# Kernel tuning notes

Measured on AMD Instinct MI355X. Metric: run time of the kernel, lower is better.

Reference implementation:

```python
import jax, jax.numpy as jnp
import numpy as np

INV_SQRT2 = 0.7071067811865476
BETA = 0.3
LN_EPS = 1e-5

B, S, P, C, TD = 128, 1024, 336, 128, 4
H1, H2, K = C // 4, C // 8, 3  # rda=4, rdb=8, ksize=3


def setup_inputs() -> dict:
    key = jax.random.key(0)
    ks = jax.random.split(key, 20)
    rn = lambda k, sh: jax.random.normal(k, sh, dtype=jnp.float32)
    return {
        "x": rn(ks[0], (B, S, C)),
        "x_mark_enc": rn(ks[1], (B, S, TD)),
        "x_dec": rn(ks[2], (B, P, C)),
        "y_mark_dec": rn(ks[3], (B, P, TD)),
        # time_enc params
        "W1": rn(ks[4], (H1, TD)) * 0.1, "b1": jnp.zeros((H1,), jnp.float32),
        "g1": jnp.ones((H1,), jnp.float32), "be1": jnp.zeros((H1,), jnp.float32),
        "W2": rn(ks[5], (H2, H1)) * 0.1, "b2": jnp.zeros((H2,), jnp.float32),
        "g2": jnp.ones((H2,), jnp.float32), "be2": jnp.zeros((H2,), jnp.float32),
        "Wc": rn(ks[6], (S, S, K)) * 0.02, "bc": jnp.zeros((S,), jnp.float32),
        "W3": rn(ks[7], (C, H2)) * 0.1, "b3": jnp.zeros((C,), jnp.float32),
        # projections
        "Wtp": rn(ks[8], (P, S)) * 0.02, "btp": jnp.zeros((P,), jnp.float32),
        "Whp": rn(ks[9], (P, S)) * 0.02, "bhp": jnp.zeros((P,), jnp.float32),
    }


def _haar_level1(x):
    # pywt.wavedec(sig, 'db1', level=1) -> [cA, cD]; concat along time.
    # For even length: cA[k]=(x[2k]+x[2k+1])/sqrt(2), cD[k]=(x[2k]-x[2k+1])/sqrt(2).
    xe, xo = x[:, 0::2, :], x[:, 1::2, :]
    cA = (xe + xo) * INV_SQRT2
    cD = (xe - xo) * INV_SQRT2
    return jnp.concatenate([cA, cD], axis=1)  # [B, S, C]


def _layernorm(h, g, b):
    m = jnp.mean(h, axis=-1, keepdims=True)
    v = jnp.mean((h - m) ** 2, axis=-1, keepdims=True)
    return (h - m) * jax.lax.rsqrt(v + LN_EPS) * g + b


def reference(x, x_mark_enc, x_dec, y_mark_dec,
              W1, b1, g1, be1, W2, b2, g2, be2, Wc, bc, W3, b3,
              Wtp, btp, Whp, bhp):
    # wavelet transform + instance norm over time (torch.var is unbiased)
    xw = _haar_level1(x)
    means = jnp.mean(xw, axis=1, keepdims=True)
    stdev = jnp.sqrt(jnp.var(xw, axis=1, ddof=1, keepdims=True) + 1e-5)
    xn = (xw - means) / stdev

    # time_enc MLP: Linear -> LN -> ReLU -> Linear -> LN -> ReLU
    h = jax.nn.relu(_layernorm(jnp.einsum('bst,ht->bsh', x_mark_enc, W1) + b1, g1, be1))
    h = jax.nn.relu(_layernorm(jnp.einsum('bsh,gh->bsg', h, W2) + b2, g2, be2))
    # Conv1d(in=seq_len, out=seq_len, k=3, padding='same') over feature dim H2
    h = jax.lax.conv_general_dilated(h, Wc, window_strides=(1,), padding='SAME',
                                     dimension_numbers=('NCH', 'OIH', 'NCH'))
    h = h + bc[None, :, None]
    time_embed = jnp.einsum('bsg,cg->bsc', h, W3) + b3  # [B, S, C]

    # seq->pred projections (Linear over time axis), then blend
    time_out = jnp.einsum('bsc,ps->bpc', time_embed, Wtp) + btp[None, :, None]
    pred = jnp.einsum('bsc,ps->bpc', xn, Whp) + bhp[None, :, None]
    pred = BETA * pred + (1.0 - BETA) * time_out
    pred = pred * stdev + means
    return pred  # [B, P, C] == dec_out[:, -pred_len:, :]
```

## Files before the change

kernel.cpp:

```cpp
#include <hip/hip_runtime.h>
#include <hip/hip_bf16.h>

#define INV_SQRT2f 0.70710678118654752440f
#define BETAf 0.3f
#define OMBf  0.7f
#define LN_EPSf 1e-5f

#define B 128
#define S 1024
#define P 336
#define C 128
#define H1 32
#define H2 16

#define WS_WHP2G  0
#define WS_EPI    262144
#define WS_BCP    296448
#define WS_H2     296832
#define WS_M      2393984
#define WS_AIMG   3426176

typedef short  s16x8 __attribute__((ext_vector_type(8)));
typedef float  f32x4 __attribute__((ext_vector_type(4)));

__device__ __forceinline__ unsigned f2bf(float f) {
    unsigned u = __float_as_uint(f);
    return (u + 0x7fffu + ((u >> 16) & 1u)) >> 16;
}

__device__ __forceinline__ int whp2l_u32(int p, int sp) {
    int kt   = sp >> 4;
    int tile = kt * 2 + p / 192;
    int sub  = (p % 192) >> 4;
    int kg   = (sp & 15) >> 2;
    int m    = p & 15;
    int byte = tile * 12288 + sub * 1024 + kg * 256 + m * 16 + 4 * (sp & 3);
    return byte >> 2;
}

__global__ void k_prep(const float* __restrict__ Whp, const float* __restrict__ Wtp,
                       const float* __restrict__ bc,  const float* __restrict__ bhp,
                       const float* __restrict__ btp, float* __restrict__ ws)
{
    const int p = blockIdx.x;
    const int t = threadIdx.x;
    unsigned* img = (unsigned*)ws;
    __shared__ float red[768];
    float sw = 0.f, rw = 0.f, bp = 0.f;
    for (int sp = t; sp < 512; sp += 256) {
        float a = Whp[p * 1024 + sp];
        float d = Whp[p * 1024 + 512 + sp];
        float va = BETAf * (a + d) * INV_SQRT2f;
        float vb = BETAf * (a - d) * INV_SQRT2f;
        img[whp2l_u32(p, sp)] = f2bf(va) | (f2bf(vb) << 16);
        sw += a + d;
    }
    for (int s = t; s < S; s += 256) {
        float w = Wtp[p * 1024 + s];
        rw += w;
        bp += w * bc[s];
    }
    red[t] = sw; red[256 + t] = rw; red[512 + t] = bp;
    __syncthreads();
    for (int off = 128; off > 0; off >>= 1) {
        if (t < off) {
            red[t]       += red[t + off];
            red[256 + t] += red[256 + t + off];
            red[512 + t] += red[512 + t + off];
        }
        __syncthreads();
    }
    if (t == 0) {
        ws[WS_BCP + p] = red[512];
        float* e = ws + WS_EPI + p * 4;
        e[0] = BETAf * bhp[p] + OMBf * btp[p];
        e[1] = OMBf * red[256];
        e[2] = 1.f - BETAf * red[0];
        e[3] = 0.f;
    }
}

__global__ void k_mlp(const float* __restrict__ xme,
                      const float* __restrict__ W1, const float* __restrict__ b1,
                      const float* __restrict__ g1, const float* __restrict__ be1,
                      const float* __restrict__ W2, const float* __restrict__ b2,
                      const float* __restrict__ g2, const float* __restrict__ be2,
                      float* __restrict__ ws)
{
    __shared__ float w1s[128], b1s[32], g1s[32], be1s[32];
    __shared__ float w2s[512], b2s[16], g2s[16], be2s[16];
    const int t = threadIdx.x;
    if (t < 128) w1s[t] = W1[t];
    if (t < 32) { b1s[t] = b1[t]; g1s[t] = g1[t]; be1s[t] = be1[t]; }
    for (int i = t; i < 512; i += 256) w2s[i] = W2[i];
    if (t < 16) { b2s[t] = b2[t]; g2s[t] = g2[t]; be2s[t] = be2[t]; }
    __syncthreads();

    const int row = blockIdx.x * 256 + t;
    float4 v = *(const float4*)(xme + (size_t)row * 4);

    float h1v[32];
    float m = 0.f;
    #pragma unroll
    for (int i = 0; i < 32; i++) {
        float a = w1s[i*4+0]*v.x + w1s[i*4+1]*v.y + w1s[i*4+2]*v.z + w1s[i*4+3]*v.w + b1s[i];
        h1v[i] = a; m += a;
    }
    m *= (1.f / 32.f);
    float var = 0.f;
    #pragma unroll
    for (int i = 0; i < 32; i++) { float d = h1v[i] - m; var += d * d; }
    var *= (1.f / 32.f);
    float rs = rsqrtf(var + LN_EPSf);
    #pragma unroll
    for (int i = 0; i < 32; i++)
        h1v[i] = fmaxf((h1v[i] - m) * rs * g1s[i] + be1s[i], 0.f);

    float h2v[16];
    float m2 = 0.f;
    #pragma unroll
    for (int g = 0; g < 16; g++) {
        float a = b2s[g];
        #pragma unroll
        for (int i = 0; i < 32; i++) a = fmaf(w2s[g * 32 + i], h1v[i], a);
        h2v[g] = a; m2 += a;
    }
    m2 *= (1.f / 16.f);
    float v2 = 0.f;
    #pragma unroll
    for (int g = 0; g < 16; g++) { float d = h2v[g] - m2; v2 += d * d; }
    v2 *= (1.f / 16.f);
    float rs2 = rsqrtf(v2 + LN_EPSf);
    float* h2o = ws + WS_H2 + (size_t)row * 16;
    #pragma unroll
    for (int g = 0; g < 16; g++)
        h2o[g] = fmaxf((h2v[g] - m2) * rs2 * g2s[g] + be2s[g], 0.f);
}

__global__ __launch_bounds__(256) void k_wcp(const float* __restrict__ Wc,
                                             const float* __restrict__ Wtp,
                                             float* __restrict__ ws)
{
    __shared__ __align__(16) unsigned short Bs[2][4][4][16][8];
    const int pbase = blockIdx.x * 96;
    const int n0    = blockIdx.y * 64;
    const int t     = threadIdx.x;
    const int lane  = t & 63;
    const int wid   = t >> 6;
    const int wm    = wid >> 1;
    const int wn    = wid & 1;
    const int g8    = lane >> 4;
    const int n16   = lane & 15;

    const int bn  = t & 63;
    const int bkg = t >> 6;

    int prow[3];
    #pragma unroll
    for (int fi = 0; fi < 3; fi++) {
        int pr = pbase + wm * 48 + fi * 16 + n16;
        prow[fi] = pr < P ? pr : P - 1;
    }

#define LOADB_(dst, kt) {                                                   \
    const float* xs_ = Wc + (size_t)((kt) * 32 + 8 * bkg) * 3072 + n0 + bn; \
    _Pragma("unroll")                                                       \
    for (int e_ = 0; e_ < 8; e_++) dst[e_] = xs_[(size_t)e_ * 3072]; }

#define WRITEB_(src, buf) {                                                 \
    uint4 w_;                                                               \
    w_.x = f2bf(src[0]) | (f2bf(src[1]) << 16);                             \
    w_.y = f2bf(src[2]) | (f2bf(src[3]) << 16);                             \
    w_.z = f2bf(src[4]) | (f2bf(src[5]) << 16);                             \
    w_.w = f2bf(src[6]) | (f2bf(src[7]) << 16);                             \
    *(uint4*)&Bs[buf][bn >> 4][bkg][bn & 15][0] = w_; }

#define LOADA_(dst, kt) {                                                   \
    _Pragma("unroll")                                                       \
    for (int fi_ = 0; fi_ < 3; fi_++) {                                     \
        const float* as_ = Wtp + (size_t)prow[fi_] * 1024 + (kt) * 32 + g8 * 8; \
        dst[fi_][0] = *(const float4*)(as_);                                \
        dst[fi_][1] = *(const float4*)(as_ + 4); } }

#define PACKA_(fa, src) {                                                   \
    _Pragma("unroll")                                                       \
    for (int fi_ = 0; fi_ < 3; fi_++) {                                     \
        uint4 w_;                                                           \
        w_.x = f2bf(src[fi_][0].x) | (f2bf(src[fi_][0].y) << 16);           \
        w_.y = f2bf(src[fi_][0].z) | (f2bf(src[fi_][0].w) << 16);           \
        w_.z = f2bf(src[fi_][1].x) | (f2bf(src[fi_][1].y) << 16);           \
        w_.w = f2bf(src[fi_][1].z) | (f2bf(src[fi_][1].w) << 16);           \
        fa[fi_] = *(s16x8*)&w_; } }

#define MFMA6_(buf, fa) {                                                   \
    s16x8 fb0 = *(const s16x8*)&Bs[buf][2 * wn + 0][g8][n16][0];            \
    s16x8 fb1 = *(const s16x8*)&Bs[buf][2 * wn + 1][g8][n16][0];            \
    _Pragma("unroll")                                                       \
    for (int fi_ = 0; fi_ < 3; fi_++) {                                     \
        acc[fi_][0] = __builtin_amdgcn_mfma_f32_16x16x32_bf16(fa[fi_], fb0, acc[fi_][0], 0, 0, 0); \
        acc[fi_][1] = __builtin_amdgcn_mfma_f32_16x16x32_bf16(fa[fi_], fb1, acc[fi_][1], 0, 0, 0); } }

    f32x4 acc[3][2];
    #pragma unroll
    for (int i = 0; i < 3; i++) {
        acc[i][0] = (f32x4){0.f, 0.f, 0.f, 0.f};
        acc[i][1] = (f32x4){0.f, 0.f, 0.f, 0.f};
    }

    float  b0r[8], b1r[8];
    float4 a0r[3][2], a1r[3][2];

    LOADA_(a0r, 0); LOADB_(b0r, 0);
    LOADA_(a1r, 1); LOADB_(b1r, 1);
    WRITEB_(b0r, 0);
    __syncthreads();

    for (int i = 0; i < 16; i++) {
        const int kt = 2 * i;
        {
            s16x8 fa[3];
            PACKA_(fa, a0r);
            if (kt + 2 < 32) { LOADA_(a0r, kt + 2); LOADB_(b0r, kt + 2); }
            MFMA6_(0, fa);
        }
        __syncthreads();
        WRITEB_(b1r, 1);
        __syncthreads();
        {
            s16x8 fa[3];
            PACKA_(fa, a1r);
            if (kt + 3 < 32) { LOADA_(a1r, kt + 3); LOADB_(b1r, kt + 3); }
            MFMA6_(1, fa);
        }
        __syncthreads();
        if (kt + 2 < 32) WRITEB_(b0r, 0);
        __syncthreads();
    }

#undef LOADB_
#undef WRITEB_
#undef LOADA_
#undef PACKA_
#undef MFMA6_

    unsigned short* aimg16 = (unsigned short*)(ws + WS_AIMG);
    #pragma unroll
    for (int fi = 0; fi < 3; fi++) {
        #pragma unroll
        for (int q = 0; q < 2; q++) {
            const int m3 = n0 + wn * 32 + q * 16 + n16;
            const int iq = m3 / 3;
            const int k  = m3 - 3 * iq;
            const int ch = k * 32 + (iq >> 5);
            const int lh = ((iq >> 3) & 3) << 4;
            const int e  = iq & 7;
            #pragma unroll
            for (int r = 0; r < 4; r++) {
                const int p  = pbase + wm * 48 + fi * 16 + g8 * 4 + r;
                const int pf = p >> 4;
                const int l  = lh | (p & 15);
                unsigned short v = (p < P) ? (unsigned short)f2bf(acc[fi][q][r])
                                           : (unsigned short)0;
                aimg16[((size_t)(ch * 24 + pf) * 64 + l) * 8 + e] = v;
            }
        }
    }
}

#define HT_RS 1056
__global__ __launch_bounds__(256) void k_mconv(float* __restrict__ ws)
{
    __shared__ unsigned short Ht[18 * HT_RS];
    const int b  = blockIdx.x;
    const int pt = blockIdx.y;
    const int t  = threadIdx.x;
    const int l  = t & 63;
    const int wid = t >> 6;
    const int pf = pt * 4 + wid;
    const int n16 = l & 15;
    const int g8  = l >> 4;

    for (int j = t; j < HT_RS; j += 256) {
        Ht[j] = 0;
        Ht[17 * HT_RS + j] = 0;
    }
    {
        const float* h2b = ws + WS_H2 + (size_t)b * 16384;
        const int s0 = t * 4;
        float v[4][16];
        #pragma unroll
        for (int rr = 0; rr < 4; rr++) {
            const float4* src = (const float4*)(h2b + (size_t)(s0 + rr) * 16);
            float4 a0 = src[0], a1 = src[1], a2 = src[2], a3 = src[3];
            v[rr][0]=a0.x; v[rr][1]=a0.y; v[rr][2]=a0.z; v[rr][3]=a0.w;
            v[rr][4]=a1.x; v[rr][5]=a1.y; v[rr][6]=a1.z; v[rr][7]=a1.w;
            v[rr][8]=a2.x; v[rr][9]=a2.y; v[rr][10]=a2.z; v[rr][11]=a2.w;
            v[rr][12]=a3.x; v[rr][13]=a3.y; v[rr][14]=a3.z; v[rr][15]=a3.w;
        }
        #pragma unroll
        for (int g = 0; g < 16; g++) {
            uint2 w;
            w.x = f2bf(v[0][g]) | (f2bf(v[1][g]) << 16);
            w.y = f2bf(v[2][g]) | (f2bf(v[3][g]) << 16);
            *(uint2*)&Ht[(g + 1) * HT_RS + s0] = w;
        }
    }
    __syncthreads();

    const uint4* ab = (const uint4*)(ws + WS_AIMG);
    const size_t lidx = (size_t)pf * 64 + l;
    f32x4 acc = (f32x4){0.f, 0.f, 0.f, 0.f};

    uint4 nf0 = ab[lidx + (size_t)0 * 1536];
    uint4 nf1 = ab[lidx + (size_t)1 * 1536];
    uint4 nf2 = ab[lidx + (size_t)2 * 1536];
    uint4 nf3 = ab[lidx + (size_t)3 * 1536];

    for (int g = 0; g < 24; g++) {
        uint4 c0 = nf0, c1 = nf1, c2 = nf2, c3 = nf3;
        if (g < 23) {
            const size_t nb = lidx + (size_t)(g + 1) * 4 * 1536;
            nf0 = ab[nb];
            nf1 = ab[nb + 1536];
            nf2 = ab[nb + 2 * 1536];
            nf3 = ab[nb + 3 * 1536];
        }
        #pragma unroll
        for (int e = 0; e < 4; e++) {
            const int it = 4 * g + e;
            const int k  = it >> 5;
            const int kt = it & 31;
            s16x8 fb = *(const s16x8*)&Ht[(n16 + k) * HT_RS + kt * 32 + g8 * 8];
            uint4 ce = (e == 0) ? c0 : (e == 1) ? c1 : (e == 2) ? c2 : c3;
            s16x8 fa = *(s16x8*)&ce;
            acc = __builtin_amdgcn_mfma_f32_16x16x32_bf16(fa, fb, acc, 0, 0, 0);
        }
    }

    #pragma unroll
    for (int r = 0; r < 4; r++) {
        int p = pf * 16 + g8 * 4 + r;
        if (p < P)
            ws[WS_M + ((size_t)b * P + p) * 16 + n16] = acc[r] + ws[WS_BCP + p];
    }
}

__global__ __launch_bounds__(256, 2) void k_pred(
    const float* __restrict__ x,
    const float* __restrict__ W3, const float* __restrict__ b3,
    const float* __restrict__ ws, float* __restrict__ out)
{
    __shared__ __align__(16) unsigned short Bs[2][4][4][16][8];
    __shared__ float sev[256], ssq[256], smean[64], sstd[64];
    const int b     = blockIdx.x;
    const int pt    = blockIdx.y;
    const int ptile = pt >> 1;
    const int chalf = pt & 1;
    const int t     = threadIdx.x;
    const int lane  = t & 63;
    const int wm    = t >> 6;
    const int g8    = lane >> 4;
    const int n16   = lane & 15;

    const int sc  = t & 63;
    const int skg = t >> 6;

    const float* xb = x + (size_t)b * S * C + chalf * 64;
    const char* aimgc = (const char*)ws + ptile * 12288
        + (wm * 3) * 1024 + g8 * 256 + n16 * 16;

    f32x4 acc[3][4];
    #pragma unroll
    for (int i = 0; i < 3; i++)
        #pragma unroll
        for (int j = 0; j < 4; j++) acc[i][j] = (f32x4){0.f, 0.f, 0.f, 0.f};

    float ev_acc = 0.f, sq_acc = 0.f;

#define P_LOADB_(dst, kt) {                                                 \
    const float* xs_ = xb + (size_t)(32 * (kt) + 8 * skg) * C + sc;         \
    _Pragma("unroll")                                                       \
    for (int e_ = 0; e_ < 8; e_++) dst[e_] = xs_[(size_t)e_ * C]; }

#define P_WRITEB_(src, buf) {                                               \
    uint4 w_;                                                               \
    w_.x = f2bf(src[0]) | (f2bf(src[1]) << 16);                             \
    w_.y = f2bf(src[2]) | (f2bf(src[3]) << 16);                             \
    w_.z = f2bf(src[4]) | (f2bf(src[5]) << 16);                             \
    w_.w = f2bf(src[6]) | (f2bf(src[7]) << 16);                             \
    *(uint4*)&Bs[buf][sc >> 4][skg][sc & 15][0] = w_;                       \
    _Pragma("unroll")                                                       \
    for (int e_ = 0; e_ < 8; e_++) {                                        \
        float v_ = src[e_];                                                 \
        sq_acc = fmaf(v_, v_, sq_acc);                                      \
        if ((e_ & 1) == 0) ev_acc += v_;    \
    } }

#define P_LOADA_(dst, kt) {                                                 \
    const char* ap_ = aimgc + (size_t)(kt) * 24576;                         \
    _Pragma("unroll")                                                       \
    for (int fi_ = 0; fi_ < 3; fi_++)                                       \
        dst[fi_] = *(const uint4*)(ap_ + fi_ * 1024); }

#define P_MFMA_(buf, au) {                                                  \
    s16x8 fb0 = *(const s16x8*)&Bs[buf][0][g8][n16][0];                     \
    s16x8 fb1 = *(const s16x8*)&Bs[buf][1][g8][n16][0];                     \
    s16x8 fb2 = *(const s16x8*)&Bs[buf][2][g8][n16][0];                     \
    s16x8 fb3 = *(const s16x8*)&Bs[buf][3][g8][n16][0];                     \
    _Pragma("unroll")                                                       \
    for (int fi_ = 0; fi_ < 3; fi_++) {                                     \
        s16x8 fa_ = *(s16x8*)&au[fi_];                                      \
        acc[fi_][0] = __builtin_amdgcn_mfma_f32_16x16x32_bf16(fa_, fb0, acc[fi_][0], 0, 0, 0); \
        acc[fi_][1] = __builtin_amdgcn_mfma_f32_16x16x32_bf16(fa_, fb1, acc[fi_][1], 0, 0, 0); \
        acc[fi_][2] = __builtin_amdgcn_mfma_f32_16x16x32_bf16(fa_, fb2, acc[fi_][2], 0, 0, 0); \
        acc[fi_][3] = __builtin_amdgcn_mfma_f32_16x16x32_bf16(fa_, fb3, acc[fi_][3], 0, 0, 0); } }

    float b0r[8], b1r[8];
    uint4 a0u[3], a1u[3];

    P_LOADB_(b0r, 0); P_LOADB_(b1r, 1);
    P_LOADA_(a0u, 0); P_LOADA_(a1u, 1);
    P_WRITEB_(b0r, 0);
    __syncthreads();

    for (int i = 0; i < 16; i++) {
        const int kt = 2 * i;
        {
            uint4 au[3];
            #pragma unroll
            for (int fi = 0; fi < 3; fi++) au[fi] = a0u[fi];
            if (kt + 2 < 32) { P_LOADA_(a0u, kt + 2); P_LOADB_(b0r, kt + 2); }
            P_MFMA_(0, au);
            P_WRITEB_(b1r, 1);
            __syncthreads();
        }
        {
            const int kt1 = kt + 1;
            uint4 au[3];
            #pragma unroll
            for (int fi = 0; fi < 3; fi++) au[fi] = a1u[fi];
            if (kt1 + 2 < 32) { P_LOADA_(a1u, kt1 + 2); P_LOADB_(b1r, kt1 + 2); }
            P_MFMA_(1, au);
            if (kt1 < 31) P_WRITEB_(b0r, 0);
            __syncthreads();
        }
    }

#undef P_LOADB_
#undef P_WRITEB_
#undef P_LOADA_
#undef P_MFMA_

    sev[t] = ev_acc; ssq[t] = sq_acc;
    __syncthreads();
    if (t < 64) {
        float ev = sev[t] + sev[t + 64] + sev[t + 128] + sev[t + 192];
        float sq = ssq[t] + ssq[t + 64] + ssq[t + 128] + ssq[t + 192];
        float mean = ev * (INV_SQRT2f / 512.f);
        float var  = (sq - 1024.f * mean * mean) * (1.f / 1023.f);
        smean[t] = mean;
        sstd[t]  = sqrtf(var + LN_EPSf);
    }
    __syncthreads();

    float sdv[4], mnv[4], b3v[4];
    f32x4 w3r[4][4];
    #pragma unroll
    for (int fj = 0; fj < 4; fj++) {
        int cl = fj * 16 + n16;
        int c  = chalf * 64 + cl;
        sdv[fj] = sstd[cl];
        mnv[fj] = smean[cl];
        b3v[fj] = b3[c];
        const f32x4* wr = (const f32x4*)(W3 + c * 16);
        #pragma unroll
        for (int q = 0; q < 4; q++) w3r[fj][q] = wr[q];
    }
    const int prow0 = ptile * 192 + wm * 48 + g8 * 4;
    #pragma unroll
    for (int fi = 0; fi < 3; fi++) {
        #pragma unroll
        for (int r = 0; r < 4; r++) {
            int p  = prow0 + fi * 16 + r;
            int pc = p < P ? p : P - 1;
            const f32x4* mrow = (const f32x4*)(ws + WS_M + ((size_t)b * P + pc) * 16);
            f32x4 m0 = mrow[0], m1 = mrow[1], m2 = mrow[2], m3 = mrow[3];
            const float* e = ws + WS_EPI + pc * 4;
            float A13 = e[0], A4 = e[1], A2 = e[2];
            #pragma unroll
            for (int fj = 0; fj < 4; fj++) {
                float s = 0.f;
                #pragma unroll
                for (int q = 0; q < 4; q++) {
                    const f32x4 mv = (q==0)?m0:(q==1)?m1:(q==2)?m2:m3;
                    s = fmaf(mv.x, w3r[fj][q].x, s);
                    s = fmaf(mv.y, w3r[fj][q].y, s);
                    s = fmaf(mv.z, w3r[fj][q].z, s);
                    s = fmaf(mv.w, w3r[fj][q].w, s);
                }
                float res = acc[fi][fj][r]
                          + sdv[fj] * (OMBf * s + A13 + A4 * b3v[fj])
                          + A2 * mnv[fj];
                if (p < P)
                    out[((size_t)b * P + p) * C + chalf * 64 + fj * 16 + n16] = res;
            }
        }
    }
}

extern "C" void kernel_launch(void* const* d_in, const int* in_sizes, int n_in,
                              void* d_out, int out_size, void* d_ws, size_t ws_size,
                              hipStream_t stream)
{
    const float* x    = (const float*)d_in[0];
    const float* xme  = (const float*)d_in[1];
    const float* W1   = (const float*)d_in[4];
    const float* b1   = (const float*)d_in[5];
    const float* g1   = (const float*)d_in[6];
    const float* be1  = (const float*)d_in[7];
    const float* W2   = (const float*)d_in[8];
    const float* b2   = (const float*)d_in[9];
    const float* g2   = (const float*)d_in[10];
    const float* be2  = (const float*)d_in[11];
    const float* Wc   = (const float*)d_in[12];
    const float* bc   = (const float*)d_in[13];
    const float* W3   = (const float*)d_in[14];
    const float* b3   = (const float*)d_in[15];
    const float* Wtp  = (const float*)d_in[16];
    const float* btp  = (const float*)d_in[17];
    const float* Whp  = (const float*)d_in[18];
    const float* bhp  = (const float*)d_in[19];
    float* ws  = (float*)d_ws;
    float* out = (float*)d_out;

    k_prep  <<<dim3(P),      dim3(256), 0, stream>>>(Whp, Wtp, bc, bhp, btp, ws);
    k_mlp   <<<dim3(512),    dim3(256), 0, stream>>>(xme, W1, b1, g1, be1,
                                                     W2, b2, g2, be2, ws);
    k_wcp   <<<dim3(4, 48),  dim3(256), 0, stream>>>(Wc, Wtp, ws);
    k_mconv <<<dim3(B, 6),   dim3(256), 0, stream>>>(ws);
    k_pred  <<<dim3(B, 4),   dim3(256), 0, stream>>>(x, W3, b3, ws, out);
}
```

Measured before the change: 96.53 us.

## Pre-convert x to bf16 MFMA image and split out instance-norm statistics

Adds a k_xc kernel that reads x once, converts it to bf16 in the exact MFMA B-fragment layout in workspace, and writes partial sums for the mean and variance. A small k_stats2 kernel then reduces those into per-(b,c) mean and std. k_pred now loads B fragments straight from global memory with a 3-stage register prefetch, with no LDS staging and no barriers. Previously each of the two p-tiles re-read and re-converted x. The change costs two extra launches and a round trip of about 32MB of bf16 image through workspace.

Result: slower. 115.0 us (+19.2%).

```diff
diff --git a/kernel.cpp b/kernel.cpp
--- a/kernel.cpp
+++ b/kernel.cpp
@@ -19,6 +19,11 @@
 #define WS_H2     296832
 #define WS_M      2393984
 #define WS_AIMG   3426176
+#define WS_XIMG   4194304
+#define WS_EVP    12582912
+#define WS_SQP    13107200
+#define WS_MEAN   13631488
+#define WS_STD    13647872
 
 typedef short  s16x8 __attribute__((ext_vector_type(8)));
 typedef float  f32x4 __attribute__((ext_vector_type(4)));
@@ -135,6 +140,63 @@
     #pragma unroll
     for (int g = 0; g < 16; g++)
         h2o[g] = fmaxf((h2v[g] - m2) * rs2 * g2s[g] + be2s[g], 0.f);
+}
+
+__global__ __launch_bounds__(256) void k_xc(const float* __restrict__ x,
+                                            float* __restrict__ ws)
+{
+    __shared__ float sev[256], ssq[256];
+    const int b  = blockIdx.x;
+    const int kt = blockIdx.y;
+    const int t  = threadIdx.x;
+    const int c  = t & 127;
+    const int h  = t >> 7;
+    const float* xb = x + (size_t)b * S * C + (size_t)(32 * kt) * C + c;
+    char* ximg = (char*)(ws + WS_XIMG);
+
+    float ev = 0.f, sq = 0.f;
+    #pragma unroll
+    for (int j = 0; j < 2; j++) {
+        const int kg = 2 * h + j;
+        const float* xs = xb + (size_t)(8 * kg) * C;
+        float v[8];
+        #pragma unroll
+        for (int e = 0; e < 8; e++) v[e] = xs[(size_t)e * C];
+        uint4 w;
+        w.x = f2bf(v[0]) | (f2bf(v[1]) << 16);
+        w.y = f2bf(v[2]) | (f2bf(v[3]) << 16);
+        w.z = f2bf(v[4]) | (f2bf(v[5]) << 16);
+        w.w = f2bf(v[6]) | (f2bf(v[7]) << 16);
+        #pragma unroll
+        for (int e = 0; e < 8; e++) {
+            sq = fmaf(v[e], v[e], sq);
+            if ((e & 1) == 0) ev += v[e];
+        }
+        char* dst = ximg + ((size_t)((b * 2 + (c >> 6)) * 32 + kt)) * 4096
+                  + ((((c & 63) >> 4) * 4 + kg) << 8) + ((c & 15) << 4);
+        *(uint4*)dst = w;
+    }
+    sev[t] = ev; ssq[t] = sq;
+    __syncthreads();
+    if (t < 128) {
+        ws[WS_EVP + ((size_t)b * 32 + kt) * 128 + t] = sev[t] + sev[t + 128];
+        ws[WS_SQP + ((size_t)b * 32 + kt) * 128 + t] = ssq[t] + ssq[t + 128];
+    }
+}
+
+__global__ void k_stats2(float* __restrict__ ws)
+{
+    const int idx = blockIdx.x * 256 + threadIdx.x;
+    const int b = idx >> 7, c = idx & 127;
+    float ev = 0.f, sq = 0.f;
+    for (int j = 0; j < 32; j++) {
+        ev += ws[WS_EVP + ((size_t)b * 32 + j) * 128 + c];
+        sq += ws[WS_SQP + ((size_t)b * 32 + j) * 128 + c];
+    }
+    float mean = ev * (INV_SQRT2f / 512.f);
+    float var  = (sq - 1024.f * mean * mean) * (1.f / 1023.f);
+    ws[WS_MEAN + idx] = mean;
+    ws[WS_STD + idx]  = sqrtf(var + LN_EPSf);
 }
 
 __global__ __launch_bounds__(256) void k_wcp(const float* __restrict__ Wc,
@@ -346,12 +408,9 @@
 }
 
 __global__ __launch_bounds__(256, 2) void k_pred(
-    const float* __restrict__ x,
     const float* __restrict__ W3, const float* __restrict__ b3,
     const float* __restrict__ ws, float* __restrict__ out)
 {
-    __shared__ __align__(16) unsigned short Bs[2][4][4][16][8];
-    __shared__ float sev[256], ssq[256], smean[64], sstd[64];
     const int b     = blockIdx.x;
     const int pt    = blockIdx.y;
     const int ptile = pt >> 1;
@@ -362,39 +421,16 @@
     const int g8    = lane >> 4;
     const int n16   = lane & 15;
 
-    const int sc  = t & 63;
-    const int skg = t >> 6;
-
-    const float* xb = x + (size_t)b * S * C + chalf * 64;
     const char* aimgc = (const char*)ws + ptile * 12288
         + (wm * 3) * 1024 + g8 * 256 + n16 * 16;
+    const char* bimgc = (const char*)(ws + WS_XIMG)
+        + ((size_t)(b * 2 + chalf) * 32) * 4096 + (g8 << 8) + (n16 << 4);
 
     f32x4 acc[3][4];
     #pragma unroll
     for (int i = 0; i < 3; i++)
         #pragma unroll
         for (int j = 0; j < 4; j++) acc[i][j] = (f32x4){0.f, 0.f, 0.f, 0.f};
-
-    float ev_acc = 0.f, sq_acc = 0.f;
-
-#define P_LOADB_(dst, kt) {                                                 \
-    const float* xs_ = xb + (size_t)(32 * (kt) + 8 * skg) * C + sc;         \
-    _Pragma("unroll")                                                       \
-    for (int e_ = 0; e_ < 8; e_++) dst[e_] = xs_[(size_t)e_ * C]; }
-
-#define P_WRITEB_(src, buf) {                                               \
-    uint4 w_;                                                               \
-    w_.x = f2bf(src[0]) | (f2bf(src[1]) << 16);                             \
-    w_.y = f2bf(src[2]) | (f2bf(src[3]) << 16);                             \
-    w_.z = f2bf(src[4]) | (f2bf(src[5]) << 16);                             \
-    w_.w = f2bf(src[6]) | (f2bf(src[7]) << 16);                             \
-    *(uint4*)&Bs[buf][sc >> 4][skg][sc & 15][0] = w_;                       \
-    _Pragma("unroll")                                                       \
-    for (int e_ = 0; e_ < 8; e_++) {                                        \
-        float v_ = src[e_];                                                 \
-        sq_acc = fmaf(v_, v_, sq_acc);                                      \
-        if ((e_ & 1) == 0) ev_acc += v_;    \
-    } }
 
 #define P_LOADA_(dst, kt) {                                                 \
     const char* ap_ = aimgc + (size_t)(kt) * 24576;                         \
@@ -402,75 +438,59 @@
     for (int fi_ = 0; fi_ < 3; fi_++)                                       \
         dst[fi_] = *(const uint4*)(ap_ + fi_ * 1024); }
 
-#define P_MFMA_(buf, au) {                                                  \
-    s16x8 fb0 = *(const s16x8*)&Bs[buf][0][g8][n16][0];                     \
-    s16x8 fb1 = *(const s16x8*)&Bs[buf][1][g8][n16][0];                     \
-    s16x8 fb2 = *(const s16x8*)&Bs[buf][2][g8][n16][0];                     \
-    s16x8 fb3 = *(const s16x8*)&Bs[buf][3][g8][n16][0];                     \
+#define P_LOADB_(dst, kt) {                                                 \
+    const char* bp_ = bimgc + (size_t)(kt) * 4096;                          \
+    _Pragma("unroll")                                                       \
+    for (int fj_ = 0; fj_ < 4; fj_++)                                       \
+        dst[fj_] = *(const uint4*)(bp_ + fj_ * 1024); }
+
+#define P_MFMA_(ca, cb) {                                                   \
     _Pragma("unroll")                                                       \
     for (int fi_ = 0; fi_ < 3; fi_++) {                                     \
-        s16x8 fa_ = *(s16x8*)&au[fi_];                                      \
-        acc[fi_][0] = __builtin_amdgcn_mfma_f32_16x16x32_bf16(fa_, fb0, acc[fi_][0], 0, 0, 0); \
-        acc[fi_][1] = __builtin_amdgcn_mfma_f32_16x16x32_bf16(fa_, fb1, acc[fi_][1], 0, 0, 0); \
-        acc[fi_][2] = __builtin_amdgcn_mfma_f32_16x16x32_bf16(fa_, fb2, acc[fi_][2], 0, 0, 0); \
-        acc[fi_][3] = __builtin_amdgcn_mfma_f32_16x16x32_bf16(fa_, fb3, acc[fi_][3], 0, 0, 0); } }
-
-    float b0r[8], b1r[8];
-    uint4 a0u[3], a1u[3];
-
-    P_LOADB_(b0r, 0); P_LOADB_(b1r, 1);
-    P_LOADA_(a0u, 0); P_LOADA_(a1u, 1);
-    P_WRITEB_(b0r, 0);
-    __syncthreads();
-
-    for (int i = 0; i < 16; i++) {
-        const int kt = 2 * i;
-        {
-            uint4 au[3];
-            #pragma unroll
-            for (int fi = 0; fi < 3; fi++) au[fi] = a0u[fi];
-            if (kt + 2 < 32) { P_LOADA_(a0u, kt + 2); P_LOADB_(b0r, kt + 2); }
-            P_MFMA_(0, au);
-            P_WRITEB_(b1r, 1);
-            __syncthreads();
-        }
-        {
-            const int kt1 = kt + 1;
-            uint4 au[3];
-            #pragma unroll
-            for (int fi = 0; fi < 3; fi++) au[fi] = a1u[fi];
-            if (kt1 + 2 < 32) { P_LOADA_(a1u, kt1 + 2); P_LOADB_(b1r, kt1 + 2); }
-            P_MFMA_(1, au);
-            if (kt1 < 31) P_WRITEB_(b0r, 0);
-            __syncthreads();
-        }
-    }
-
+        s16x8 fa_ = *(s16x8*)&ca[fi_];                                      \
+        _Pragma("unroll")                                                   \
+        for (int fj_ = 0; fj_ < 4; fj_++) {                                 \
+            s16x8 fb_ = *(s16x8*)&cb[fj_];                                  \
+            acc[fi_][fj_] = __builtin_amdgcn_mfma_f32_16x16x32_bf16(        \
+                fa_, fb_, acc[fi_][fj_], 0, 0, 0); } } }
+
+#define P_STEP_(kt, SA, SB) {                                               \
+    if ((kt) < 32) {                                                        \
+        uint4 ca_[3], cb_[4];                                               \
+        ca_[0] = SA[0]; ca_[1] = SA[1]; ca_[2] = SA[2];                     \
+        cb_[0] = SB[0]; cb_[1] = SB[1]; cb_[2] = SB[2]; cb_[3] = SB[3];     \
+        if ((kt) + 3 < 32) { P_LOADA_(SA, (kt) + 3); P_LOADB_(SB, (kt) + 3); } \
+        P_MFMA_(ca_, cb_);                                                  \
+    } }
+
+    uint4 s0a[3], s0b[4], s1a[3], s1b[4], s2a[3], s2b[4];
+
+    P_LOADA_(s0a, 0); P_LOADB_(s0b, 0);
+    P_LOADA_(s1a, 1); P_LOADB_(s1b, 1);
+    P_LOADA_(s2a, 2); P_LOADB_(s2b, 2);
+
+    for (int i6 = 0; i6 < 6; i6++) {
+        const int k0 = 6 * i6;
+        P_STEP_(k0 + 0, s0a, s0b);
+        P_STEP_(k0 + 1, s1a, s1b);
+        P_STEP_(k0 + 2, s2a, s2b);
+        P_STEP_(k0 + 3, s0a, s0b);
+        P_STEP_(k0 + 4, s1a, s1b);
+        P_STEP_(k0 + 5, s2a, s2b);
+    }
+
+#undef P_STEP_
+#undef P_LOADA_
 #undef P_LOADB_
-#undef P_WRITEB_
-#undef P_LOADA_
 #undef P_MFMA_
-
-    sev[t] = ev_acc; ssq[t] = sq_acc;
-    __syncthreads();
-    if (t < 64) {
-        float ev = sev[t] + sev[t + 64] + sev[t + 128] + sev[t + 192];
-        float sq = ssq[t] + ssq[t + 64] + ssq[t + 128] + ssq[t + 192];
-        float mean = ev * (INV_SQRT2f / 512.f);
-        float var  = (sq - 1024.f * mean * mean) * (1.f / 1023.f);
-        smean[t] = mean;
-        sstd[t]  = sqrtf(var + LN_EPSf);
-    }
-    __syncthreads();
 
     float sdv[4], mnv[4], b3v[4];
     f32x4 w3r[4][4];
     #pragma unroll
     for (int fj = 0; fj < 4; fj++) {
-        int cl = fj * 16 + n16;
-        int c  = chalf * 64 + cl;
-        sdv[fj] = sstd[cl];
-        mnv[fj] = smean[cl];
+        int c = chalf * 64 + fj * 16 + n16;
+        sdv[fj] = ws[WS_STD  + b * C + c];
+        mnv[fj] = ws[WS_MEAN + b * C + c];
         b3v[fj] = b3[c];
         const f32x4* wr = (const f32x4*)(W3 + c * 16);
         #pragma unroll
@@ -536,7 +556,9 @@
     k_prep  <<<dim3(P),      dim3(256), 0, stream>>>(Whp, Wtp, bc, bhp, btp, ws);
     k_mlp   <<<dim3(512),    dim3(256), 0, stream>>>(xme, W1, b1, g1, be1,
                                                      W2, b2, g2, be2, ws);
+    k_xc    <<<dim3(B, 32),  dim3(256), 0, stream>>>(x, ws);
+    k_stats2<<<dim3(64),     dim3(256), 0, stream>>>(ws);
     k_wcp   <<<dim3(4, 48),  dim3(256), 0, stream>>>(Wc, Wtp, ws);
     k_mconv <<<dim3(B, 6),   dim3(256), 0, stream>>>(ws);
-    k_pred  <<<dim3(B, 4),   dim3(256), 0, stream>>>(x, W3, b3, ws, out);
-}
+    k_pred  <<<dim3(B, 4),   dim3(256), 0, stream>>>(W3, b3, ws, out);
+}
```
